# Performance work log

Measured on AMD Instinct MI355X. Metric: run time of the kernel, lower is better.

The kernel has to match this reference:

```python
import jax, jax.numpy as jnp
import numpy as np


def setup_inputs() -> dict:
    key = jax.random.key(0)
    k1, k2, k3, k4 = jax.random.split(key, 4)
    B, S, D = 2, 2048, 1024
    return {
        "X": jax.random.normal(k1, (B, S, D), dtype=jnp.float32),
        "W_q": jax.random.normal(k2, (D, D), dtype=jnp.float32),
        "W_k": jax.random.normal(k3, (D, D), dtype=jnp.float32),
        "W_v": jax.random.normal(k4, (D, D), dtype=jnp.float32),
        "n_heads": 16,
    }


def reference(X, W_q, W_k, W_v, n_heads):
    B, S, D = X.shape
    H = n_heads
    dh = D // H
    # QKV projections, split heads: [B,S,D] -> [H,B,S,dh]
    def split_heads(Y):
        return Y.reshape(B, S, H, dh).transpose(2, 0, 1, 3)
    Q = split_heads(X @ W_q)
    K = split_heads(X @ W_k)
    V = split_heads(X @ W_v)
    scale = 1.0 / jnp.sqrt(jnp.asarray(dh, dtype=X.dtype))
    # [H,B,S,S] attention scores (naive, matches the original)
    scores = jax.nn.softmax(jnp.einsum("hbqd,hbkd->hbqk", Q, K) * scale, axis=-1)
    out = jnp.einsum("hbqk,hbkd->hbqd", scores, V)  # [H,B,S,dh]
    # torch.concat(out, 0) over leading H dim -> [H*B, S, dh]
    return out.reshape(H * B, S, dh)
```

## Files before the change

kernel.cpp:

```cpp
#include <hip/hip_runtime.h>

typedef unsigned short u16;
typedef unsigned int u32;
typedef __bf16 bf16x8 __attribute__((ext_vector_type(8)));
typedef float f32x4 __attribute__((ext_vector_type(4)));
typedef float f32x16 __attribute__((ext_vector_type(16)));

extern "C" __device__ float __ocml_native_exp2_f32(float);

#define WT_HI_E  ((size_t)0)
#define WT_LO_E  ((size_t)3 << 20)
#define X_HI_E   ((size_t)6 << 20)
#define X_LO_E   ((size_t)10 << 20)
#define Q_HI_E   ((size_t)14 << 20)
#define Q_LO_E   ((size_t)18 << 20)
#define K_HI_E   ((size_t)22 << 20)
#define K_LO_E   ((size_t)26 << 20)
#define V_HI_E   ((size_t)30 << 20)

__device__ __forceinline__ u16 bf16_rne(float x) {
  u32 u = __float_as_uint(x);
  u32 r = (u + 0x7fffu + ((u >> 16) & 1u)) >> 16;
  return (u16)r;
}
__device__ __forceinline__ float bf16_f(u16 h) {
  return __uint_as_float(((u32)h) << 16);
}
__device__ __forceinline__ u16 f2bf(float x) {
  __bf16 b = (__bf16)x;
  return __builtin_bit_cast(u16, b);
}

__device__ __forceinline__ void gload16(const u16* g, u16* l) {
  __builtin_amdgcn_global_load_lds(
      (const __attribute__((address_space(1))) void*)g,
      (__attribute__((address_space(3))) void*)l, 16, 0, 0);
}

__global__ __launch_bounds__(256) void k_split(const float* __restrict__ X,
                                               const float* __restrict__ w0,
                                               const float* __restrict__ w1,
                                               const float* __restrict__ w2,
                                               u16* __restrict__ ws) {
  int bid = blockIdx.x;
  if (bid < 2048) {
    u16* xh = ws + X_HI_E;
    u16* xl = ws + X_LO_E;
    size_t i = ((size_t)bid * 256 + threadIdx.x) * 8;
    float4 a = *(const float4*)(X + i);
    float4 b = *(const float4*)(X + i + 4);
    float v[8] = {a.x, a.y, a.z, a.w, b.x, b.y, b.z, b.w};
    u32 Hh[4], Ll[4];
#pragma unroll
    for (int j = 0; j < 4; j++) {
      u16 h0 = f2bf(v[2 * j]);
      u16 h1 = f2bf(v[2 * j + 1]);
      u16 l0 = f2bf(v[2 * j] - bf16_f(h0));
      u16 l1 = f2bf(v[2 * j + 1] - bf16_f(h1));
      Hh[j] = (u32)h0 | ((u32)h1 << 16);
      Ll[j] = (u32)l0 | ((u32)l1 << 16);
    }
    *(uint4*)(xh + i) = make_uint4(Hh[0], Hh[1], Hh[2], Hh[3]);
    *(uint4*)(xl + i) = make_uint4(Ll[0], Ll[1], Ll[2], Ll[3]);
  } else {
    int wb = bid - 2048;
    int z = wb >> 8;
    int rem = wb & 255;
    int by = (rem >> 4) * 64, bx = (rem & 15) * 64;
    const float* W = (z == 0) ? w0 : ((z == 1) ? w1 : w2);
    u16* th = ws + WT_HI_E + (size_t)z * (1u << 20);
    u16* tl = ws + WT_LO_E + (size_t)z * (1u << 20);
    __shared__ float tile[64][65];
    int tx = threadIdx.x & 15, ty = threadIdx.x >> 4;
#pragma unroll
    for (int i = 0; i < 4; i++) {
      int r = ty + i * 16;
      float4 v = *(const float4*)(W + (size_t)(by + r) * 1024 + bx + tx * 4);
      tile[r][tx * 4 + 0] = v.x;
      tile[r][tx * 4 + 1] = v.y;
      tile[r][tx * 4 + 2] = v.z;
      tile[r][tx * 4 + 3] = v.w;
    }
    __syncthreads();
#pragma unroll
    for (int p = 0; p < 2; p++) {
      int t = threadIdx.x + 256 * p;
      int kc = t & 7, nl = t >> 3;
      u32 Hh[4], Ll[4];
#pragma unroll
      for (int u = 0; u < 4; u++) {
        float v0 = tile[kc * 8 + 2 * u][nl];
        float v1 = tile[kc * 8 + 2 * u + 1][nl];
        u16 h0 = f2bf(v0);
        u16 h1 = f2bf(v1);
        u16 l0 = f2bf(v0 - bf16_f(h0));
        u16 l1 = f2bf(v1 - bf16_f(h1));
        Hh[u] = (u32)h0 | ((u32)h1 << 16);
        Ll[u] = (u32)l0 | ((u32)l1 << 16);
      }
      size_t o = (size_t)(bx + nl) * 1024 + by + kc * 8;
      *(uint4*)(th + o) = make_uint4(Hh[0], Hh[1], Hh[2], Hh[3]);
      *(uint4*)(tl + o) = make_uint4(Ll[0], Ll[1], Ll[2], Ll[3]);
    }
  }
}

__global__ __launch_bounds__(256, 4) void k_proj(u16* __restrict__ ws) {
  int id = blockIdx.x;
  int xcd = id & 7;
  int loc = id >> 3;
  int m_loc = loc & 7;
  int rest = loc >> 3;
  int n_blk = rest & 7, z = rest >> 3;
  int M0 = (xcd * 8 + m_loc) * 64;
  int N0 = n_blk * 128;

  const u16* Xh = ws + X_HI_E;
  const u16* Xl = ws + X_LO_E;
  const u16* Wh = ws + WT_HI_E + (size_t)z * (1u << 20);
  const u16* Wl = ws + WT_LO_E + (size_t)z * (1u << 20);
  u16* dsth = ws + ((z == 0) ? Q_HI_E : ((z == 1) ? K_HI_E : V_HI_E));
  u16* dstl = (z == 0) ? (ws + Q_LO_E) : ((z == 1) ? (ws + K_LO_E) : (u16*)0);

  __shared__ u16 smem[12288];
  u16* sXh = smem;
  u16* sXl = smem + 2048;
  u16* sWh = smem + 4096;
  u16* sWl = smem + 8192;

  int tid = threadIdx.x, lane = tid & 63, w = tid >> 6;
  int quad = lane >> 4, l16 = lane & 15;
  int mb = (w & 1) * 32, nb = (w >> 1) * 64;

  const f32x4 z4 = {0.f, 0.f, 0.f, 0.f};
  f32x4 acc[4][2];
#pragma unroll
  for (int j = 0; j < 4; j++)
#pragma unroll
    for (int i = 0; i < 2; i++) acc[j][i] = z4;

  int xrow = tid >> 2, xq8 = tid & 3;

  for (int kk = 0; kk < 1024; kk += 32) {
    __syncthreads();
    {
      size_t gx = (size_t)(M0 + xrow) * 1024 + kk + xq8 * 8;
      gload16(Xh + gx, &sXh[(size_t)(w * 16) * 32]);
      if (z != 2) gload16(Xl + gx, &sXl[(size_t)(w * 16) * 32]);
#pragma unroll
      for (int j = 0; j < 2; j++) {
        int c = tid + 256 * j;
        int row = c >> 2, q8 = c & 3;
        size_t gw = (size_t)(N0 + row) * 1024 + kk + q8 * 8;
        gload16(Wh + gw, &sWh[(size_t)(j * 64 + w * 16) * 32]);
        if (z != 2) gload16(Wl + gw, &sWl[(size_t)(j * 64 + w * 16) * 32]);
      }
    }
    __syncthreads();
    bf16x8 ah[2], bh[4];
#pragma unroll
    for (int i = 0; i < 2; i++)
      ah[i] = *(const bf16x8*)&sXh[(mb + i * 16 + l16) * 32 + quad * 8];
#pragma unroll
    for (int j = 0; j < 4; j++)
      bh[j] = *(const bf16x8*)&sWh[(nb + j * 16 + l16) * 32 + quad * 8];
    if (z != 2) {
      bf16x8 al[2], bl[4];
#pragma unroll
      for (int i = 0; i < 2; i++)
        al[i] = *(const bf16x8*)&sXl[(mb + i * 16 + l16) * 32 + quad * 8];
#pragma unroll
      for (int j = 0; j < 4; j++)
        bl[j] = *(const bf16x8*)&sWl[(nb + j * 16 + l16) * 32 + quad * 8];
#pragma unroll
      for (int j = 0; j < 4; j++)
#pragma unroll
        for (int i = 0; i < 2; i++) {
          f32x4 c0 = acc[j][i];
          c0 = __builtin_amdgcn_mfma_f32_16x16x32_bf16(bh[j], ah[i], c0, 0, 0, 0);
          c0 = __builtin_amdgcn_mfma_f32_16x16x32_bf16(bh[j], al[i], c0, 0, 0, 0);
          c0 = __builtin_amdgcn_mfma_f32_16x16x32_bf16(bl[j], ah[i], c0, 0, 0, 0);
          acc[j][i] = c0;
        }
    } else {
#pragma unroll
      for (int j = 0; j < 4; j++)
#pragma unroll
        for (int i = 0; i < 2; i++)
          acc[j][i] = __builtin_amdgcn_mfma_f32_16x16x32_bf16(ah[i], bh[j], acc[j][i], 0, 0, 0);
    }
  }

  __syncthreads();
  int b = M0 >> 11, S0 = M0 & 2047;

  if (z != 2) {
    u16* my = smem + (size_t)w * 2048;
    int hh = (N0 + nb) >> 6;
    int sbase = S0 + mb;
    float qscale = (z == 0) ? (0.125f * 1.4426950408889634f) : 1.0f;
#pragma unroll
    for (int pass = 0; pass < 2; pass++) {
      u16* dst = pass ? dstl : dsth;
#pragma unroll
      for (int j = 0; j < 4; j++)
#pragma unroll
        for (int i = 0; i < 2; i++) {
          int dl = j * 16 + quad * 4;
          int sl = i * 16 + l16;
          u16 e[4];
#pragma unroll
          for (int r = 0; r < 4; r++) {
            float y = acc[j][i][r] * qscale;
            u16 hv = bf16_rne(y);
            e[r] = pass ? bf16_rne(y - bf16_f(hv)) : hv;
          }
          int elem = sl * 64 + (((dl >> 3) ^ (sl & 7)) << 3) + (dl & 7);
          *(uint2*)&my[elem] = make_uint2((u32)e[0] | ((u32)e[1] << 16),
                                          (u32)e[2] | ((u32)e[3] << 16));
        }
#pragma unroll
      for (int t = 0; t < 4; t++) {
        int sr = (lane >> 3) + t * 8;
        int p = lane & 7;
        int rc = (z == 1) ? p : (p ^ (sr & 7));
        uint4 v = *(const uint4*)&my[sr * 64 + rc * 8];
        size_t o = ((size_t)(hh * 2 + b) * 2048 + sbase + sr) * 64 + p * 8;
        *(uint4*)&dst[o] = v;
      }
    }
  } else {
#pragma unroll
    for (int j = 0; j < 4; j++)
#pragma unroll
      for (int i = 0; i < 2; i++) {
        int dl = j * 16 + l16;
        int s64 = mb + i * 16 + quad * 4;
        u16 e[4];
#pragma unroll
        for (int r = 0; r < 4; r++) e[r] = bf16_rne(acc[j][i][r]);
        int cp = ((s64 >> 3) & 7) ^ (dl & 7);
        int elem = (w >> 1) * 4096 + dl * 64 + (cp << 3) + (s64 & 7);
        *(uint2*)&smem[elem] = make_uint2((u32)e[0] | ((u32)e[1] << 16),
                                          (u32)e[2] | ((u32)e[3] << 16));
      }
    __syncthreads();
    int half = w >> 1;
    int hh = (N0 + half * 64) >> 6;
#pragma unroll
    for (int t = 0; t < 4; t++) {
      int dr = (w & 1) * 32 + (lane >> 3) + t * 8;
      int p = lane & 7;
      uint4 v = *(const uint4*)&smem[half * 4096 + dr * 64 + p * 8];
      size_t o = ((size_t)(hh * 2 + b) * 64 + dr) * 2048 + S0 + p * 8;
      *(uint4*)&dsth[o] = v;
    }
  }
}

__global__ __launch_bounds__(256, 2) void k_attn(u16* __restrict__ ws,
                                                 float* __restrict__ out) {
  const u16* Qh = ws + Q_HI_E;
  const u16* Ql = ws + Q_LO_E;
  const u16* Kh = ws + K_HI_E;
  const u16* Kl = ws + K_LO_E;
  const u16* Vt = ws + V_HI_E;

  __shared__ u16 sKh[3][64][64], sKl[3][64][64], sVt[3][64][64];

  int id = blockIdx.x;
  int hb = id & 31, qb = id >> 5;
  int tid = threadIdx.x, w = tid >> 6, lane = tid & 63;
  int l31 = lane & 31, h = lane >> 5;
  size_t base = (size_t)hb * (2048 * 64);
  int qw0 = qb * 128 + w * 32;

  int srow = lane >> 3, sch = lane & 7;

  auto stage = [&](int buf, int kt) {
#pragma unroll
    for (int b2 = 0; b2 < 2; b2++) {
      int rr = w * 16 + b2 * 8;
      size_t kg = base + (size_t)(kt + rr + srow) * 64 + sch * 8;
      gload16(Kh + kg, &sKh[buf][rr][0]);
      gload16(Kl + kg, &sKl[buf][rr][0]);
      size_t vg = base + (size_t)(rr + srow) * 2048 + kt + sch * 8;
      gload16(Vt + vg, &sVt[buf][rr][0]);
    }
  };

  stage(0, 0);
  stage(1, 64);

  bf16x8 qh[4], ql[4];
#pragma unroll
  for (int ks = 0; ks < 4; ks++) {
    size_t off = base + (size_t)(qw0 + l31) * 64 + ks * 16 + h * 8;
    qh[ks] = *(const bf16x8*)(Qh + off);
    ql[ks] = *(const bf16x8*)(Ql + off);
  }

  auto rdA = [&](const u16 t[64][64], int mt, int ks) -> bf16x8 {
    int ch = ((ks * 2 + h) ^ (l31 & 7)) * 8;
    return *(const bf16x8*)&t[mt * 32 + l31][ch];
  };

  auto qkt = [&](int buf, f32x16* sc) {
#pragma unroll
    for (int i = 0; i < 16; i++) { sc[0][i] = 0.f; sc[1][i] = 0.f; }
    __builtin_amdgcn_s_setprio(1);
#pragma unroll
    for (int ks = 0; ks < 4; ks++)
#pragma unroll
      for (int mt = 0; mt < 2; mt++) {
        bf16x8 kh = rdA(sKh[buf], mt, ks);
        bf16x8 kl = rdA(sKl[buf], mt, ks);
        sc[mt] = __builtin_amdgcn_mfma_f32_32x32x16_bf16(kh, qh[ks], sc[mt], 0, 0, 0);
        sc[mt] = __builtin_amdgcn_mfma_f32_32x32x16_bf16(kh, ql[ks], sc[mt], 0, 0, 0);
        sc[mt] = __builtin_amdgcn_mfma_f32_32x32x16_bf16(kl, qh[ks], sc[mt], 0, 0, 0);
      }
    __builtin_amdgcn_s_setprio(0);
  };

  f32x16 o[2];
#pragma unroll
  for (int i = 0; i < 16; i++) { o[0][i] = 0.f; o[1][i] = 0.f; }
  float mr = -1e30f, lr = 0.f;

  f32x16 scA[2], scB[2];

  __syncthreads();
  qkt(0, scA);

  auto body = [&](int it, f32x16* scc, f32x16* scn) {
    __syncthreads();
    if (it + 2 < 32) stage((it + 2) % 3, (it + 2) * 64);
    if (it + 1 < 32) qkt((it + 1) % 3, scn);

    float m8[8];
#pragma unroll
    for (int i = 0; i < 8; i++)
      m8[i] = fmaxf(fmaxf(scc[0][2 * i], scc[0][2 * i + 1]),
                    fmaxf(scc[1][2 * i], scc[1][2 * i + 1]));
#pragma unroll
    for (int s = 4; s > 0; s >>= 1)
#pragma unroll
      for (int i = 0; i < 4; i++)
        if (i < s) m8[i] = fmaxf(m8[i], m8[i + s]);
    float mx = fmaxf(m8[0], __shfl_xor(m8[0], 32));
    if (!__all(mx - mr <= 8.0f)) {
      float mnew = fmaxf(mr, mx);
      float alpha = __ocml_native_exp2_f32(mr - mnew);
      mr = mnew;
      lr *= alpha;
#pragma unroll
      for (int i = 0; i < 16; i++) { o[0][i] *= alpha; o[1][i] *= alpha; }
    }
    float rs = 0.f;
    u32 pk[2][8];
#pragma unroll
    for (int t = 0; t < 2; t++)
#pragma unroll
      for (int i = 0; i < 8; i++) {
        float p0 = __ocml_native_exp2_f32(scc[t][2 * i] - mr);
        float p1 = __ocml_native_exp2_f32(scc[t][2 * i + 1] - mr);
        rs += p0 + p1;
        u32 a = __float_as_uint(p0) + 0x8000u;
        u32 b = __float_as_uint(p1) + 0x8000u;
        pk[t][i] = __builtin_amdgcn_perm(b, a, 0x07060302u);
      }
    rs += __shfl_xor(rs, 32);
    lr += rs;

    int buf = it % 3;
    __builtin_amdgcn_s_setprio(1);
#pragma unroll
    for (int ks = 0; ks < 4; ks++) {
      int t = ks >> 1, c = ks & 1;
      u32 b0 = pk[t][c * 4 + 0], b1 = pk[t][c * 4 + 1];
      u32 b2 = pk[t][c * 4 + 2], b3 = pk[t][c * 4 + 3];
      u32 rA = (u32)__shfl_xor((int)(h ? b0 : b2), 32);
      u32 rB = (u32)__shfl_xor((int)(h ? b1 : b3), 32);
      uint4 fb = h ? make_uint4(rA, rB, b2, b3) : make_uint4(b0, b1, rA, rB);
      bf16x8 pfrag = *(bf16x8*)&fb;
#pragma unroll
      for (int mt = 0; mt < 2; mt++) {
        bf16x8 vb = rdA(sVt[buf], mt, ks);
        o[mt] = __builtin_amdgcn_mfma_f32_32x32x16_bf16(vb, pfrag, o[mt], 0, 0, 0);
      }
    }
    __builtin_amdgcn_s_setprio(0);
  };

  for (int it = 0; it < 32; it += 2) {
    body(it, scA, scB);
    body(it + 1, scB, scA);
  }

  float inv = 1.f / lr;
  size_t grow = (size_t)hb * 2048 + qw0 + l31;
#pragma unroll
  for (int mt = 0; mt < 2; mt++)
#pragma unroll
    for (int g2 = 0; g2 < 4; g2++) {
      int d0 = mt * 32 + g2 * 8 + 4 * h;
      float4 v = make_float4(o[mt][g2 * 4 + 0] * inv, o[mt][g2 * 4 + 1] * inv,
                             o[mt][g2 * 4 + 2] * inv, o[mt][g2 * 4 + 3] * inv);
      *(float4*)(out + grow * 64 + d0) = v;
    }
}

extern "C" void kernel_launch(void* const* d_in, const int* in_sizes, int n_in,
                              void* d_out, int out_size, void* d_ws, size_t ws_size,
                              hipStream_t stream) {
  const float* X = (const float*)d_in[0];
  const float* Wq = (const float*)d_in[1];
  const float* Wk = (const float*)d_in[2];
  const float* Wv = (const float*)d_in[3];
  u16* ws = (u16*)d_ws;
  float* out = (float*)d_out;

  k_split<<<dim3(2816), dim3(256), 0, stream>>>(X, Wq, Wk, Wv, ws);
  k_proj<<<dim3(1536), dim3(256), 0, stream>>>(ws);
  k_attn<<<dim3(512), dim3(256), 0, stream>>>(ws, out);
}
```

Before: 229.8 us.

## Deepen attention K/V prefetch to three tiles with vmcnt-based waits

Prefetch now runs three key tiles ahead instead of two. K/K-lo keep three LDS buffers, and V gets a fourth so the V tile still in use is never overwritten. The full __syncthreads before each iteration becomes an explicit s_waitcnt vmcnt that waits only for the oldest tile, followed by a raw s_barrier, so later loads can stay in flight. Total LDS per block rises to 80KB, which leaves little headroom for two blocks per CU. The counter-based waits also depend on the exact number of outstanding loads per stage.

```diff
diff --git a/kernel.cpp b/kernel.cpp
--- a/kernel.cpp
+++ b/kernel.cpp
@@ -266,7 +266,7 @@
   const u16* Kl = ws + K_LO_E;
   const u16* Vt = ws + V_HI_E;
 
-  __shared__ u16 sKh[3][64][64], sKl[3][64][64], sVt[3][64][64];
+  __shared__ u16 sKh[3][64][64], sKl[3][64][64], sVt[4][64][64];
 
   int id = blockIdx.x;
   int hb = id & 31, qb = id >> 5;
@@ -277,20 +277,18 @@
 
   int srow = lane >> 3, sch = lane & 7;
 
-  auto stage = [&](int buf, int kt) {
+  auto stage = [&](int n) {
+    int kb = n % 3, vb = n & 3, kt = n * 64;
 #pragma unroll
     for (int b2 = 0; b2 < 2; b2++) {
       int rr = w * 16 + b2 * 8;
       size_t kg = base + (size_t)(kt + rr + srow) * 64 + sch * 8;
-      gload16(Kh + kg, &sKh[buf][rr][0]);
-      gload16(Kl + kg, &sKl[buf][rr][0]);
+      gload16(Kh + kg, &sKh[kb][rr][0]);
+      gload16(Kl + kg, &sKl[kb][rr][0]);
       size_t vg = base + (size_t)(rr + srow) * 2048 + kt + sch * 8;
-      gload16(Vt + vg, &sVt[buf][rr][0]);
+      gload16(Vt + vg, &sVt[vb][rr][0]);
     }
   };
-
-  stage(0, 0);
-  stage(1, 64);
 
   bf16x8 qh[4], ql[4];
 #pragma unroll
@@ -300,12 +298,16 @@
     ql[ks] = *(const bf16x8*)(Ql + off);
   }
 
+  stage(0);
+  stage(1);
+  stage(2);
+
   auto rdA = [&](const u16 t[64][64], int mt, int ks) -> bf16x8 {
     int ch = ((ks * 2 + h) ^ (l31 & 7)) * 8;
     return *(const bf16x8*)&t[mt * 32 + l31][ch];
   };
 
-  auto qkt = [&](int buf, f32x16* sc) {
+  auto qkt = [&](int kb, f32x16* sc) {
 #pragma unroll
     for (int i = 0; i < 16; i++) { sc[0][i] = 0.f; sc[1][i] = 0.f; }
     __builtin_amdgcn_s_setprio(1);
@@ -313,8 +315,8 @@
     for (int ks = 0; ks < 4; ks++)
 #pragma unroll
       for (int mt = 0; mt < 2; mt++) {
-        bf16x8 kh = rdA(sKh[buf], mt, ks);
-        bf16x8 kl = rdA(sKl[buf], mt, ks);
+        bf16x8 kh = rdA(sKh[kb], mt, ks);
+        bf16x8 kl = rdA(sKl[kb], mt, ks);
         sc[mt] = __builtin_amdgcn_mfma_f32_32x32x16_bf16(kh, qh[ks], sc[mt], 0, 0, 0);
         sc[mt] = __builtin_amdgcn_mfma_f32_32x32x16_bf16(kh, ql[ks], sc[mt], 0, 0, 0);
         sc[mt] = __builtin_amdgcn_mfma_f32_32x32x16_bf16(kl, qh[ks], sc[mt], 0, 0, 0);
@@ -329,12 +331,17 @@
 
   f32x16 scA[2], scB[2];
 
-  __syncthreads();
+  asm volatile("s_waitcnt vmcnt(12)" ::: "memory");
+  __builtin_amdgcn_s_barrier();
   qkt(0, scA);
 
   auto body = [&](int it, f32x16* scc, f32x16* scn) {
-    __syncthreads();
-    if (it + 2 < 32) stage((it + 2) % 3, (it + 2) * 64);
+    if (it < 30)
+      asm volatile("s_waitcnt vmcnt(6)" ::: "memory");
+    else
+      asm volatile("s_waitcnt vmcnt(0)" ::: "memory");
+    __builtin_amdgcn_s_barrier();
+    if (it + 3 < 32) stage(it + 3);
     if (it + 1 < 32) qkt((it + 1) % 3, scn);
 
     float m8[8];
@@ -372,7 +379,7 @@
     rs += __shfl_xor(rs, 32);
     lr += rs;
 
-    int buf = it % 3;
+    int vb = it & 3;
     __builtin_amdgcn_s_setprio(1);
 #pragma unroll
     for (int ks = 0; ks < 4; ks++) {
@@ -385,8 +392,8 @@
       bf16x8 pfrag = *(bf16x8*)&fb;
 #pragma unroll
       for (int mt = 0; mt < 2; mt++) {
-        bf16x8 vb = rdA(sVt[buf], mt, ks);
-        o[mt] = __builtin_amdgcn_mfma_f32_32x32x16_bf16(vb, pfrag, o[mt], 0, 0, 0);
+        bf16x8 vbf = rdA(sVt[vb], mt, ks);
+        o[mt] = __builtin_amdgcn_mfma_f32_32x32x16_bf16(vbf, pfrag, o[mt], 0, 0, 0);
       }
     }
     __builtin_amdgcn_s_setprio(0);
```

After: 229.9 us. Within noise of the previous version (+0.0%).
